# Kernel tuning notes

Measured on AMD Instinct MI355X. Metric: run time of the kernel, lower is better.

## Reference

```python
import jax, jax.numpy as jnp
import numpy as np
import math

N, N0, M, K, CIN, COUT, DIM = 50000, 50000, 32, 15, 64, 64, 3
POINT_INFLUENCE = 0.05
KERNEL_RADIUS = 1.5 * POINT_INFLUENCE  # _INFLUENCE_TO_RADIUS * point_influence


def setup_inputs() -> dict:
    key = jax.random.key(0)
    k1, k2, k3, k4, k5, k6 = jax.random.split(key, 6)
    query_points = jax.random.uniform(k1, (N, DIM), dtype=jnp.float32)
    support_points = jax.random.uniform(k2, (N0, DIM), dtype=jnp.float32)
    # index N0 is the shadow-neighbor index (padding for ragged neighborhoods)
    neighbors = jax.random.randint(k3, (N, M), 0, N0 + 1)
    x = jax.random.normal(k4, (N0, CIN), dtype=jnp.float32)
    # kernel point dispositions inside the kernel ball, center point at origin (fixed='center')
    kp = jax.random.normal(k5, (K, DIM), dtype=jnp.float32)
    kp = kp / jnp.linalg.norm(kp, axis=1, keepdims=True) * (KERNEL_RADIUS * 0.66)
    K_points = kp.at[0].set(0.0)
    # xavier_normal_ init for weight [K, CIN, COUT]
    std = math.sqrt(2.0 / (CIN + COUT))
    weight = jax.random.normal(k6, (K, CIN, COUT), dtype=jnp.float32) * std
    return dict(query_points=query_points, support_points=support_points,
                neighbors=neighbors, x=x, K_points=K_points, weight=weight)


def reference(query_points, support_points, neighbors, x, K_points, weight):
    # shadow point far away + zero shadow feature (handles padded neighbor index N0)
    shadow_pt = jnp.full((1, support_points.shape[1]), 1e6, support_points.dtype)
    sp = jnp.concatenate([support_points, shadow_pt], axis=0)          # [N0+1, 3]
    feats = jnp.concatenate([x, jnp.zeros((1, x.shape[1]), x.dtype)], axis=0)  # [N0+1, CIN]

    # gather & center neighborhoods: [N, M, 3]
    nb_pts = sp[neighbors] - query_points[:, None, :]

    # squared distance to each kernel point without materializing [N,M,K,3]:
    # ||n - k||^2 = ||n||^2 - 2 n.k + ||k||^2  -> [N, M, K]
    sq = (jnp.sum(nb_pts * nb_pts, axis=-1)[:, :, None]
          - 2.0 * jnp.einsum('nmd,kd->nmk', nb_pts, K_points)
          + jnp.sum(K_points * K_points, axis=-1))
    sq = jnp.maximum(sq, 0.0)

    # linear KP influence: clamp(1 - dist / point_influence, min=0) -> transpose to [N, K, M]
    all_weights = jnp.maximum(1.0 - jnp.sqrt(sq) / POINT_INFLUENCE, 0.0)
    all_weights = jnp.swapaxes(all_weights, 1, 2)                      # [N, K, M]

    nb_feats = feats[neighbors]                                        # [N, M, CIN]
    weighted = jnp.matmul(all_weights, nb_feats)                       # [N, K, CIN]
    # sum over kernel points of per-kernel-point matmuls ('sum' aggregation)
    out = jnp.einsum('nkc,kco->no', weighted, weight)                  # [N, COUT]
    return out
```

## Files before the change

### kernel.cpp

```cpp
#include <hip/hip_runtime.h>

#define N_Q   50000
#define N_S   50000
#define M_NB  32
#define K_PTS 15
#define CIN   64
#define COUT  64

__global__ __launch_bounds__(128) void kpconv_fused2(
    const float* __restrict__ query,
    const float* __restrict__ support,
    const int*   __restrict__ neighbors,
    const float* __restrict__ x,
    const float* __restrict__ kpts,
    const float* __restrict__ weight,
    float*       __restrict__ out)
{
    __shared__ float s_kx[K_PTS], s_ky[K_PTS], s_kz[K_PTS], s_kk[K_PTS];
    __shared__ float s_bc[2][CIN];

    const int tid = threadIdx.x;
    if (tid < K_PTS) {
        float kx = kpts[tid * 3 + 0];
        float ky = kpts[tid * 3 + 1];
        float kz = kpts[tid * 3 + 2];
        s_kx[tid] = kx; s_ky[tid] = ky; s_kz[tid] = kz;
        s_kk[tid] = kx * kx + ky * ky + kz * kz;
    }
    __syncthreads();

    const int wv   = tid >> 6;
    const int lane = tid & 63;
    const int base = blockIdx.x * 4 + wv * 2;
    const int h    = lane >> 5;
    const int n    = base + h;
    const int m    = lane & 31;

    const int idx = neighbors[n * M_NB + m];

    float dx = 0.f, dy = 0.f, dz = 0.f, nn = 1e30f;
    if (idx < N_S) {
        dx = support[idx * 3 + 0] - query[n * 3 + 0];
        dy = support[idx * 3 + 1] - query[n * 3 + 1];
        dz = support[idx * 3 + 2] - query[n * 3 + 2];
        nn = dx * dx + dy * dy + dz * dz;
    }

    float toutA = 0.f, toutB = 0.f;

    if (__ballot(nn < 0.0101f)) {
        for (int k = 0; k < K_PTS; ++k) {
            float w = 0.f;
            if (nn < 0.0101f) {
                float dot = dx * s_kx[k] + dy * s_ky[k] + dz * s_kz[k];
                float sq  = fmaxf(nn - 2.f * dot + s_kk[k], 0.f);
                if (sq < 0.0025f)
                    w = 1.f - sqrtf(sq) * 20.f;
            }
            const unsigned long long em = __ballot(w > 0.f);
            if (!em) continue;

            const float* wk = weight + (size_t)k * CIN * COUT;

            unsigned emA = (unsigned)(em & 0xffffffffull);
            while (emA) {
                float racc = 0.f;
                do {
                    const int src = __builtin_ctz(emA); emA &= emA - 1;
                    const float wsrc = __shfl(w,   src);
                    const int   isrc = __shfl(idx, src);
                    racc = fmaf(wsrc, x[(size_t)isrc * CIN + lane], racc);
                } while (emA);
                s_bc[wv][lane] = racc;
                asm volatile("" ::: "memory");
                float p0 = 0.f, p1 = 0.f, p2 = 0.f, p3 = 0.f;
                #pragma unroll 8
                for (int c = 0; c < CIN; c += 4) {
                    p0 = fmaf(s_bc[wv][c + 0], wk[(c + 0) * COUT + lane], p0);
                    p1 = fmaf(s_bc[wv][c + 1], wk[(c + 1) * COUT + lane], p1);
                    p2 = fmaf(s_bc[wv][c + 2], wk[(c + 2) * COUT + lane], p2);
                    p3 = fmaf(s_bc[wv][c + 3], wk[(c + 3) * COUT + lane], p3);
                }
                toutA += (p0 + p1) + (p2 + p3);
                asm volatile("" ::: "memory");
            }

            unsigned emB = (unsigned)(em >> 32);
            while (emB) {
                float racc = 0.f;
                do {
                    const int src = 32 + __builtin_ctz(emB); emB &= emB - 1;
                    const float wsrc = __shfl(w,   src);
                    const int   isrc = __shfl(idx, src);
                    racc = fmaf(wsrc, x[(size_t)isrc * CIN + lane], racc);
                } while (emB);
                s_bc[wv][lane] = racc;
                asm volatile("" ::: "memory");
                float p0 = 0.f, p1 = 0.f, p2 = 0.f, p3 = 0.f;
                #pragma unroll 8
                for (int c = 0; c < CIN; c += 4) {
                    p0 = fmaf(s_bc[wv][c + 0], wk[(c + 0) * COUT + lane], p0);
                    p1 = fmaf(s_bc[wv][c + 1], wk[(c + 1) * COUT + lane], p1);
                    p2 = fmaf(s_bc[wv][c + 2], wk[(c + 2) * COUT + lane], p2);
                    p3 = fmaf(s_bc[wv][c + 3], wk[(c + 3) * COUT + lane], p3);
                }
                toutB += (p0 + p1) + (p2 + p3);
                asm volatile("" ::: "memory");
            }
        }
    }

    out[(size_t)(base + 0) * COUT + lane] = toutA;
    out[(size_t)(base + 1) * COUT + lane] = toutB;
}

extern "C" void kernel_launch(void* const* d_in, const int* in_sizes, int n_in,
                              void* d_out, int out_size, void* d_ws, size_t ws_size,
                              hipStream_t stream) {
    const float* query     = (const float*)d_in[0];
    const float* support   = (const float*)d_in[1];
    const int*   neighbors = (const int*)  d_in[2];
    const float* x         = (const float*)d_in[3];
    const float* kpts      = (const float*)d_in[4];
    const float* weight    = (const float*)d_in[5];
    float*       out       = (float*)d_out;

    kpconv_fused2<<<N_Q / 4, 128, 0, stream>>>(
        query, support, neighbors, x, kpts, weight, out);
}
```

Measured before the change: 28.76 us.

## Use persistent grid-stride waves with software-prefetched neighbor and support loads

Replaces the one-block-per-4-queries launch with a fixed grid of 2048 blocks of 4 waves, each wave looping over query pairs in grid-stride order. Neighbor indices are prefetched two iterations ahead and support coordinates one iteration ahead, so gather latency overlaps the current pair's compute. The while loops around each half-wave's accumulation become single ifs, since one pass already drains the mask. The design adds registers and loop overhead, and a fixed grid can leave waves with uneven amounts of work.

```diff
diff --git a/kernel.cpp b/kernel.cpp
--- a/kernel.cpp
+++ b/kernel.cpp
@@ -6,8 +6,12 @@
 #define K_PTS 15
 #define CIN   64
 #define COUT  64
+#define NGROUPS (N_Q / 2)
+#define NBLOCKS 2048
+#define WPB     4
+#define NWAVES  (NBLOCKS * WPB)
 
-__global__ __launch_bounds__(128) void kpconv_fused2(
+__global__ __launch_bounds__(256) void kpconv_fused3(
     const float* __restrict__ query,
     const float* __restrict__ support,
     const int*   __restrict__ neighbors,
@@ -17,7 +21,7 @@
     float*       __restrict__ out)
 {
     __shared__ float s_kx[K_PTS], s_ky[K_PTS], s_kz[K_PTS], s_kk[K_PTS];
-    __shared__ float s_bc[2][CIN];
+    __shared__ float s_bc[WPB][CIN];
 
     const int tid = threadIdx.x;
     if (tid < K_PTS) {
@@ -31,87 +35,109 @@
 
     const int wv   = tid >> 6;
     const int lane = tid & 63;
-    const int base = blockIdx.x * 4 + wv * 2;
     const int h    = lane >> 5;
-    const int n    = base + h;
-    const int m    = lane & 31;
+    const int wid  = blockIdx.x * WPB + wv;
 
-    const int idx = neighbors[n * M_NB + m];
+    int gA   = wid;
+    int idxA = (gA < NGROUPS) ? neighbors[gA * 64 + lane] : N_S;
+    int gB   = gA + NWAVES;
+    int idxB = (gB < NGROUPS) ? neighbors[gB * 64 + lane] : N_S;
 
-    float dx = 0.f, dy = 0.f, dz = 0.f, nn = 1e30f;
-    if (idx < N_S) {
-        dx = support[idx * 3 + 0] - query[n * 3 + 0];
-        dy = support[idx * 3 + 1] - query[n * 3 + 1];
-        dz = support[idx * 3 + 2] - query[n * 3 + 2];
-        nn = dx * dx + dy * dy + dz * dz;
+    float sxA = 1e6f, syA = 1e6f, szA = 1e6f;
+    if (idxA < N_S) {
+        sxA = support[idxA * 3 + 0];
+        syA = support[idxA * 3 + 1];
+        szA = support[idxA * 3 + 2];
     }
 
-    float toutA = 0.f, toutB = 0.f;
+    for (int g = wid; g < NGROUPS; g += NWAVES) {
+        const int gNN  = g + 2 * NWAVES;
+        const int idxC = (gNN < NGROUPS) ? neighbors[gNN * 64 + lane] : N_S;
 
-    if (__ballot(nn < 0.0101f)) {
-        for (int k = 0; k < K_PTS; ++k) {
-            float w = 0.f;
-            if (nn < 0.0101f) {
-                float dot = dx * s_kx[k] + dy * s_ky[k] + dz * s_kz[k];
-                float sq  = fmaxf(nn - 2.f * dot + s_kk[k], 0.f);
-                if (sq < 0.0025f)
-                    w = 1.f - sqrtf(sq) * 20.f;
-            }
-            const unsigned long long em = __ballot(w > 0.f);
-            if (!em) continue;
+        float sxB = 1e6f, syB = 1e6f, szB = 1e6f;
+        if (idxB < N_S) {
+            sxB = support[idxB * 3 + 0];
+            syB = support[idxB * 3 + 1];
+            szB = support[idxB * 3 + 2];
+        }
 
-            const float* wk = weight + (size_t)k * CIN * COUT;
+        const int n = 2 * g + h;
+        const float dx = sxA - query[n * 3 + 0];
+        const float dy = syA - query[n * 3 + 1];
+        const float dz = szA - query[n * 3 + 2];
+        const float nn = dx * dx + dy * dy + dz * dz;
 
-            unsigned emA = (unsigned)(em & 0xffffffffull);
-            while (emA) {
-                float racc = 0.f;
-                do {
-                    const int src = __builtin_ctz(emA); emA &= emA - 1;
-                    const float wsrc = __shfl(w,   src);
-                    const int   isrc = __shfl(idx, src);
-                    racc = fmaf(wsrc, x[(size_t)isrc * CIN + lane], racc);
-                } while (emA);
-                s_bc[wv][lane] = racc;
-                asm volatile("" ::: "memory");
-                float p0 = 0.f, p1 = 0.f, p2 = 0.f, p3 = 0.f;
-                #pragma unroll 8
-                for (int c = 0; c < CIN; c += 4) {
-                    p0 = fmaf(s_bc[wv][c + 0], wk[(c + 0) * COUT + lane], p0);
-                    p1 = fmaf(s_bc[wv][c + 1], wk[(c + 1) * COUT + lane], p1);
-                    p2 = fmaf(s_bc[wv][c + 2], wk[(c + 2) * COUT + lane], p2);
-                    p3 = fmaf(s_bc[wv][c + 3], wk[(c + 3) * COUT + lane], p3);
+        float toutA = 0.f, toutB = 0.f;
+
+        if (__ballot(nn < 0.0101f)) {
+            const int idxCur = idxA;
+            for (int k = 0; k < K_PTS; ++k) {
+                float w = 0.f;
+                if (nn < 0.0101f) {
+                    float dot = dx * s_kx[k] + dy * s_ky[k] + dz * s_kz[k];
+                    float sq  = fmaxf(nn - 2.f * dot + s_kk[k], 0.f);
+                    if (sq < 0.0025f)
+                        w = 1.f - sqrtf(sq) * 20.f;
                 }
-                toutA += (p0 + p1) + (p2 + p3);
-                asm volatile("" ::: "memory");
-            }
+                const unsigned long long em = __ballot(w > 0.f);
+                if (!em) continue;
 
-            unsigned emB = (unsigned)(em >> 32);
-            while (emB) {
-                float racc = 0.f;
-                do {
-                    const int src = 32 + __builtin_ctz(emB); emB &= emB - 1;
-                    const float wsrc = __shfl(w,   src);
-                    const int   isrc = __shfl(idx, src);
-                    racc = fmaf(wsrc, x[(size_t)isrc * CIN + lane], racc);
-                } while (emB);
-                s_bc[wv][lane] = racc;
-                asm volatile("" ::: "memory");
-                float p0 = 0.f, p1 = 0.f, p2 = 0.f, p3 = 0.f;
-                #pragma unroll 8
-                for (int c = 0; c < CIN; c += 4) {
-                    p0 = fmaf(s_bc[wv][c + 0], wk[(c + 0) * COUT + lane], p0);
-                    p1 = fmaf(s_bc[wv][c + 1], wk[(c + 1) * COUT + lane], p1);
-                    p2 = fmaf(s_bc[wv][c + 2], wk[(c + 2) * COUT + lane], p2);
-                    p3 = fmaf(s_bc[wv][c + 3], wk[(c + 3) * COUT + lane], p3);
+                const float* wk = weight + (size_t)k * CIN * COUT;
+
+                unsigned emA = (unsigned)(em & 0xffffffffull);
+                if (emA) {
+                    float racc = 0.f;
+                    do {
+                        const int src = __builtin_ctz(emA); emA &= emA - 1;
+                        const float wsrc = __shfl(w,      src);
+                        const int   isrc = __shfl(idxCur, src);
+                        racc = fmaf(wsrc, x[(size_t)isrc * CIN + lane], racc);
+                    } while (emA);
+                    s_bc[wv][lane] = racc;
+                    asm volatile("" ::: "memory");
+                    float p0 = 0.f, p1 = 0.f, p2 = 0.f, p3 = 0.f;
+                    #pragma unroll 8
+                    for (int c = 0; c < CIN; c += 4) {
+                        p0 = fmaf(s_bc[wv][c + 0], wk[(c + 0) * COUT + lane], p0);
+                        p1 = fmaf(s_bc[wv][c + 1], wk[(c + 1) * COUT + lane], p1);
+                        p2 = fmaf(s_bc[wv][c + 2], wk[(c + 2) * COUT + lane], p2);
+                        p3 = fmaf(s_bc[wv][c + 3], wk[(c + 3) * COUT + lane], p3);
+                    }
+                    toutA += (p0 + p1) + (p2 + p3);
+                    asm volatile("" ::: "memory");
                 }
-                toutB += (p0 + p1) + (p2 + p3);
-                asm volatile("" ::: "memory");
+
+                unsigned emB = (unsigned)(em >> 32);
+                if (emB) {
+                    float racc = 0.f;
+                    do {
+                        const int src = 32 + __builtin_ctz(emB); emB &= emB - 1;
+                        const float wsrc = __shfl(w,      src);
+                        const int   isrc = __shfl(idxCur, src);
+                        racc = fmaf(wsrc, x[(size_t)isrc * CIN + lane], racc);
+                    } while (emB);
+                    s_bc[wv][lane] = racc;
+                    asm volatile("" ::: "memory");
+                    float p0 = 0.f, p1 = 0.f, p2 = 0.f, p3 = 0.f;
+                    #pragma unroll 8
+                    for (int c = 0; c < CIN; c += 4) {
+                        p0 = fmaf(s_bc[wv][c + 0], wk[(c + 0) * COUT + lane], p0);
+                        p1 = fmaf(s_bc[wv][c + 1], wk[(c + 1) * COUT + lane], p1);
+                        p2 = fmaf(s_bc[wv][c + 2], wk[(c + 2) * COUT + lane], p2);
+                        p3 = fmaf(s_bc[wv][c + 3], wk[(c + 3) * COUT + lane], p3);
+                    }
+                    toutB += (p0 + p1) + (p2 + p3);
+                    asm volatile("" ::: "memory");
+                }
             }
         }
+
+        out[(size_t)(2 * g + 0) * COUT + lane] = toutA;
+        out[(size_t)(2 * g + 1) * COUT + lane] = toutB;
+
+        idxA = idxB; idxB = idxC;
+        sxA = sxB; syA = syB; szA = szB;
     }
-
-    out[(size_t)(base + 0) * COUT + lane] = toutA;
-    out[(size_t)(base + 1) * COUT + lane] = toutB;
 }
 
 extern "C" void kernel_launch(void* const* d_in, const int* in_sizes, int n_in,
@@ -125,6 +151,6 @@
     const float* weight    = (const float*)d_in[5];
     float*       out       = (float*)d_out;
 
-    kpconv_fused2<<<N_Q / 4, 128, 0, stream>>>(
+    kpconv_fused3<<<NBLOCKS, 256, 0, stream>>>(
         query, support, neighbors, x, kpts, weight, out);
 }
```

Measured after the change: 35.54 us. 23.6% more time.
